# Kernel optimization log

Hardware: AMD Instinct MI355X
Metric: run time of the kernel (lower is better)

Reference implementation:

```python
import jax, jax.numpy as jnp
import numpy as np

N_NODES = 50000
N_EDGES = 500000
SQRT3_INV = 1.0 / np.sqrt(3.0).astype(np.float32)  # CG norm for 1e x 1e -> 0e
SQRT2_INV = 1.0 / np.sqrt(2.0).astype(np.float32)  # CG norm for 1e x 1e -> 1e


def setup_inputs() -> dict:
    key = jax.random.key(0)
    k1, k2, k3, k4, k5 = jax.random.split(key, 5)
    X = jax.random.normal(k1, (N_NODES, 128), dtype=jnp.float32)   # 32x0e + 32x1e
    Y = jax.random.normal(k2, (N_EDGES, 4), dtype=jnp.float32)     # 0e + 1e (edge SH)
    W = jax.random.normal(k3, (N_EDGES, 160), dtype=jnp.float32)   # 5 paths x 32 mul
    rows = jax.random.randint(k4, (N_EDGES,), 0, N_NODES, dtype=jnp.int64)  # receivers
    cols = jax.random.randint(k5, (N_EDGES,), 0, N_NODES, dtype=jnp.int64)  # senders
    return {"X": X, "Y": Y, "W": W, "rows": rows, "cols": cols}


def _edge_messages(Xj, Y, W):
    # Xj: [E,128] gathered sender features, Y: [E,4], W: [E,160]
    E = Xj.shape[0]
    x0 = Xj[:, :32]                       # [E,32]   32x0e
    x1 = Xj[:, 32:].reshape(E, 32, 3)     # [E,32,3] 32x1e
    y0 = Y[:, 0:1]                        # [E,1]    0e
    y1 = Y[:, 1:4]                        # [E,3]    1e
    w = W.reshape(E, 5, 32)               # per-path uvu weights
    # CG paths (uvu):
    p1 = w[:, 0] * x0 * y0                                     # 0e x 0e -> 0e  [E,32]
    p2 = (w[:, 1] * x0)[:, :, None] * y1[:, None, :]           # 0e x 1e -> 1e  [E,32,3]
    p3 = w[:, 2][:, :, None] * x1 * y0[:, :, None]             # 1e x 0e -> 1e  [E,32,3]
    p4 = w[:, 3] * jnp.einsum('eua,ea->eu', x1, y1) * SQRT3_INV  # 1e x 1e -> 0e [E,32]
    p5 = w[:, 4][:, :, None] * jnp.cross(x1, y1[:, None, :]) * SQRT2_INV  # 1e x 1e -> 1e
    return jnp.concatenate(
        [p1, p2.reshape(E, 96), p3.reshape(E, 96), p4, p5.reshape(E, 96)], axis=1
    )  # [E,352]


def reference(X, Y, W, rows, cols):
    # z_i = sum_{(i,j,e)} W_e (x_j (x)_CG y_e); rows = receiver i, cols = sender j
    Xj = X[cols]                              # per-edge gather [E,128]
    msg = _edge_messages(Xj, Y, W)            # [E,352]
    Z = jax.ops.segment_sum(msg, rows, num_segments=X.shape[0])  # scatter-add
    return Z
```

## Files before the change

### kernel.cpp

```cpp
#include <hip/hip_runtime.h>


#define SQRT3_INV 0.57735026918962576451f
#define SQRT2_INV 0.70710678118654752440f
#define KCAP 128

typedef __attribute__((ext_vector_type(4))) float f4;
typedef __attribute__((ext_vector_type(2))) int   i2;
struct F3 { float a, b, c; };

__global__ void scatter_bin_kernel(const int* __restrict__ rows, const int* __restrict__ cols,
                                   int* __restrict__ cnt, i2* __restrict__ slots,
                                   int* __restrict__ ovf_cnt, int* __restrict__ ovf_list,
                                   int nE) {
    int e = blockIdx.x * blockDim.x + threadIdx.x;
    if (e >= nE) return;
    int r = rows[e];
    int p = atomicAdd(&cnt[r], 1);
    if (p < KCAP) {
        i2 rec; rec.x = e; rec.y = cols[e];
        slots[(size_t)r * KCAP + p] = rec;
    } else {
        int q = atomicAdd(ovf_cnt, 1);
        ovf_list[q] = e;
    }
}

__global__ __launch_bounds__(256) void tpc_gather(
    const float* __restrict__ X,
    const float* __restrict__ Y,
    const float* __restrict__ W,
    const i2* __restrict__ slots,
    const int* __restrict__ cnt,
    float* __restrict__ Z,
    int n_nodes)
{
    int node = blockIdx.x * 8 + (threadIdx.x >> 5);
    if (node >= n_nodes) return;
    int u = threadIdx.x & 31;

    float a1 = 0.f, a2a = 0.f, a2b = 0.f, a2c = 0.f;
    float a3a = 0.f, a3b = 0.f, a3c = 0.f, a4 = 0.f;
    float a5a = 0.f, a5b = 0.f, a5c = 0.f;

    int n = cnt[node];
    if (n > KCAP) n = KCAP;
    const i2* sb = slots + (size_t)node * KCAP;

#define EDGE_BODY(EC_)                                                        \
    do {                                                                      \
        const float* We = W + (size_t)(unsigned)(EC_).x * 160;                \
        const float* Xr = X + (size_t)(unsigned)(EC_).y * 128;                \
        const f4 yv = *reinterpret_cast<const f4*>(Y + (size_t)(unsigned)(EC_).x * 4); \
        const float x0 = Xr[u];                                               \
        const F3 x1 = *reinterpret_cast<const F3*>(Xr + 32 + 3 * u);          \
        const float x1a = x1.a, x1b = x1.b, x1c = x1.c;                       \
        const float y0 = yv.x, y1a = yv.y, y1b = yv.z, y1c = yv.w;            \
        const float w0 = __builtin_nontemporal_load(We + u);                  \
        const float w1 = __builtin_nontemporal_load(We + 32 + u);             \
        const float w2 = __builtin_nontemporal_load(We + 64 + u);             \
        const float w3 = __builtin_nontemporal_load(We + 96 + u);             \
        const float w4 = __builtin_nontemporal_load(We + 128 + u);            \
        a1 += w0 * x0 * y0;                                                   \
        const float w1x0 = w1 * x0;                                           \
        a2a += w1x0 * y1a; a2b += w1x0 * y1b; a2c += w1x0 * y1c;              \
        const float w2y0 = w2 * y0;                                           \
        a3a += w2y0 * x1a; a3b += w2y0 * x1b; a3c += w2y0 * x1c;              \
        const float dot = x1a * y1a + x1b * y1b + x1c * y1c;                  \
        a4 += w3 * dot * SQRT3_INV;                                           \
        const float w4s = w4 * SQRT2_INV;                                     \
        a5a += w4s * (x1b * y1c - x1c * y1b);                                 \
        a5b += w4s * (x1c * y1a - x1a * y1c);                                 \
        a5c += w4s * (x1a * y1b - x1b * y1a);                                 \
    } while (0)

    int i = 0;
    for (; i + 1 < n; i += 2) {
        const i2 ec0 = sb[i];
        const i2 ec1 = sb[i + 1];
        EDGE_BODY(ec0);
        EDGE_BODY(ec1);
    }
    if (i < n) {
        const i2 ec0 = sb[i];
        EDGE_BODY(ec0);
    }
#undef EDGE_BODY

    float* Zr = Z + (size_t)node * 352;
    __builtin_nontemporal_store(a1,  Zr + u);
    __builtin_nontemporal_store(a2a, Zr + 32 + 3 * u + 0);
    __builtin_nontemporal_store(a2b, Zr + 32 + 3 * u + 1);
    __builtin_nontemporal_store(a2c, Zr + 32 + 3 * u + 2);
    __builtin_nontemporal_store(a3a, Zr + 128 + 3 * u + 0);
    __builtin_nontemporal_store(a3b, Zr + 128 + 3 * u + 1);
    __builtin_nontemporal_store(a3c, Zr + 128 + 3 * u + 2);
    __builtin_nontemporal_store(a4,  Zr + 224 + u);
    __builtin_nontemporal_store(a5a, Zr + 256 + 3 * u + 0);
    __builtin_nontemporal_store(a5b, Zr + 256 + 3 * u + 1);
    __builtin_nontemporal_store(a5c, Zr + 256 + 3 * u + 2);
}

__global__ void ovf_kernel(const float* __restrict__ X, const float* __restrict__ Y,
                           const float* __restrict__ W, const int* __restrict__ rows,
                           const int* __restrict__ cols, const int* __restrict__ ovf_cnt,
                           const int* __restrict__ ovf_list, float* __restrict__ Z) {
    const int total = ovf_cnt[0] * 32;
    for (int idx = blockIdx.x * blockDim.x + threadIdx.x; idx < total;
         idx += gridDim.x * blockDim.x) {
        const int e = ovf_list[idx >> 5];
        const int u = idx & 31;
        const int r = rows[e];
        const int c = cols[e];
        const float* Xr = X + (size_t)c * 128;
        const float x0 = Xr[u];
        const float x1a = Xr[32 + 3 * u], x1b = Xr[33 + 3 * u], x1c = Xr[34 + 3 * u];
        const float* Ye = Y + (size_t)e * 4;
        const float y0 = Ye[0], y1a = Ye[1], y1b = Ye[2], y1c = Ye[3];
        const float* We = W + (size_t)e * 160;
        const float w0 = We[u], w1 = We[32 + u], w2 = We[64 + u], w3 = We[96 + u], w4 = We[128 + u];
        const float w1x0 = w1 * x0;
        const float w2y0 = w2 * y0;
        const float dot = x1a * y1a + x1b * y1b + x1c * y1c;
        const float w4s = w4 * SQRT2_INV;
        float* Zr = Z + (size_t)r * 352;
        atomicAdd(&Zr[u], w0 * x0 * y0);
        atomicAdd(&Zr[32 + 3 * u + 0], w1x0 * y1a);
        atomicAdd(&Zr[32 + 3 * u + 1], w1x0 * y1b);
        atomicAdd(&Zr[32 + 3 * u + 2], w1x0 * y1c);
        atomicAdd(&Zr[128 + 3 * u + 0], w2y0 * x1a);
        atomicAdd(&Zr[128 + 3 * u + 1], w2y0 * x1b);
        atomicAdd(&Zr[128 + 3 * u + 2], w2y0 * x1c);
        atomicAdd(&Zr[224 + u], w3 * dot * SQRT3_INV);
        atomicAdd(&Zr[256 + 3 * u + 0], w4s * (x1b * y1c - x1c * y1b));
        atomicAdd(&Zr[256 + 3 * u + 1], w4s * (x1c * y1a - x1a * y1c));
        atomicAdd(&Zr[256 + 3 * u + 2], w4s * (x1a * y1b - x1b * y1a));
    }
}

__global__ __launch_bounds__(256) void tpc_edge_kernel(
    const float* __restrict__ X, const float* __restrict__ Y, const float* __restrict__ W,
    const int* __restrict__ rows, const int* __restrict__ cols, float* __restrict__ Z, int n_edges)
{
    int gid = blockIdx.x * blockDim.x + threadIdx.x;
    int e = gid >> 5;
    int u = gid & 31;
    if (e >= n_edges) return;
    const int r = rows[e];
    const int c = cols[e];
    const float* Xr = X + (size_t)c * 128;
    const float x0 = Xr[u];
    const float x1a = Xr[32 + 3 * u], x1b = Xr[33 + 3 * u], x1c = Xr[34 + 3 * u];
    const float* Ye = Y + (size_t)e * 4;
    const float y0 = Ye[0], y1a = Ye[1], y1b = Ye[2], y1c = Ye[3];
    const float* We = W + (size_t)e * 160;
    const float w0 = We[u], w1 = We[32 + u], w2 = We[64 + u], w3 = We[96 + u], w4 = We[128 + u];
    const float w1x0 = w1 * x0;
    const float w2y0 = w2 * y0;
    const float dot = x1a * y1a + x1b * y1b + x1c * y1c;
    const float w4s = w4 * SQRT2_INV;
    float* Zr = Z + (size_t)r * 352;
    atomicAdd(&Zr[u], w0 * x0 * y0);
    atomicAdd(&Zr[32 + 3 * u + 0], w1x0 * y1a);
    atomicAdd(&Zr[32 + 3 * u + 1], w1x0 * y1b);
    atomicAdd(&Zr[32 + 3 * u + 2], w1x0 * y1c);
    atomicAdd(&Zr[128 + 3 * u + 0], w2y0 * x1a);
    atomicAdd(&Zr[128 + 3 * u + 1], w2y0 * x1b);
    atomicAdd(&Zr[128 + 3 * u + 2], w2y0 * x1c);
    atomicAdd(&Zr[224 + u], w3 * dot * SQRT3_INV);
    atomicAdd(&Zr[256 + 3 * u + 0], w4s * (x1b * y1c - x1c * y1b));
    atomicAdd(&Zr[256 + 3 * u + 1], w4s * (x1c * y1a - x1a * y1c));
    atomicAdd(&Zr[256 + 3 * u + 2], w4s * (x1a * y1b - x1b * y1a));
}

extern "C" void kernel_launch(void* const* d_in, const int* in_sizes, int n_in,
                              void* d_out, int out_size, void* d_ws, size_t ws_size,
                              hipStream_t stream) {
    const float* X    = (const float*)d_in[0];
    const float* Y    = (const float*)d_in[1];
    const float* W    = (const float*)d_in[2];
    const int*   rows = (const int*)d_in[3];
    const int*   cols = (const int*)d_in[4];
    float* Z = (float*)d_out;

    const int n_edges = in_sizes[3];
    const int n_nodes = in_sizes[0] / 128;

    size_t slots_bytes = (size_t)n_nodes * KCAP * sizeof(i2);
    size_t need = slots_bytes + (size_t)(n_nodes + 1 + n_edges) * sizeof(int);
    if (ws_size < need) {
        hipMemsetAsync(d_out, 0, (size_t)out_size * sizeof(float), stream);
        const long long threads_total = (long long)n_edges * 32;
        const int grid = (int)((threads_total + 255) / 256);
        tpc_edge_kernel<<<grid, 256, 0, stream>>>(X, Y, W, rows, cols, Z, n_edges);
        return;
    }

    char* base = (char*)d_ws;
    i2*  slots   = (i2*)base;
    int* cnt     = (int*)(base + slots_bytes);
    int* ovf_cnt = cnt + n_nodes;
    int* ovf_list= ovf_cnt + 1;

    hipMemsetAsync(cnt, 0, (size_t)(n_nodes + 1) * sizeof(int), stream);

    const int gE = (n_edges + 255) / 256;
    scatter_bin_kernel<<<gE, 256, 0, stream>>>(rows, cols, cnt, slots, ovf_cnt, ovf_list, n_edges);

    const int gG = (n_nodes + 7) / 8;
    tpc_gather<<<gG, 256, 0, stream>>>(X, Y, W, slots, cnt, Z, n_nodes);

    ovf_kernel<<<64, 256, 0, stream>>>(X, Y, W, rows, cols, ovf_cnt, ovf_list, Z);
}
```

Measured before the change: 142.4 us.

## Split each node's edges across two half-wavefronts and reduce with shuffles

The gather kernel now assigns a full 64-lane wavefront per node instead of 32 lanes. The two halves process alternating edges and combine their partial sums with a cross-half shuffle before one half writes the output. This doubles the number of in-flight edge loads per node, aiming to hide gather latency on irregular degree lists. KCAP drops from 128 to 64, which shrinks the slot buffer, and the overflow counter is folded into the count array. In exchange, the launch needs twice as many waves and adds a shuffle reduction per output.

```diff
diff --git a/kernel.cpp b/kernel.cpp
--- a/kernel.cpp
+++ b/kernel.cpp
@@ -3,49 +3,11 @@
 
 #define SQRT3_INV 0.57735026918962576451f
 #define SQRT2_INV 0.70710678118654752440f
-#define KCAP 128
+#define KCAP 64
 
 typedef __attribute__((ext_vector_type(4))) float f4;
 typedef __attribute__((ext_vector_type(2))) int   i2;
 struct F3 { float a, b, c; };
-
-__global__ void scatter_bin_kernel(const int* __restrict__ rows, const int* __restrict__ cols,
-                                   int* __restrict__ cnt, i2* __restrict__ slots,
-                                   int* __restrict__ ovf_cnt, int* __restrict__ ovf_list,
-                                   int nE) {
-    int e = blockIdx.x * blockDim.x + threadIdx.x;
-    if (e >= nE) return;
-    int r = rows[e];
-    int p = atomicAdd(&cnt[r], 1);
-    if (p < KCAP) {
-        i2 rec; rec.x = e; rec.y = cols[e];
-        slots[(size_t)r * KCAP + p] = rec;
-    } else {
-        int q = atomicAdd(ovf_cnt, 1);
-        ovf_list[q] = e;
-    }
-}
-
-__global__ __launch_bounds__(256) void tpc_gather(
-    const float* __restrict__ X,
-    const float* __restrict__ Y,
-    const float* __restrict__ W,
-    const i2* __restrict__ slots,
-    const int* __restrict__ cnt,
-    float* __restrict__ Z,
-    int n_nodes)
-{
-    int node = blockIdx.x * 8 + (threadIdx.x >> 5);
-    if (node >= n_nodes) return;
-    int u = threadIdx.x & 31;
-
-    float a1 = 0.f, a2a = 0.f, a2b = 0.f, a2c = 0.f;
-    float a3a = 0.f, a3b = 0.f, a3c = 0.f, a4 = 0.f;
-    float a5a = 0.f, a5b = 0.f, a5c = 0.f;
-
-    int n = cnt[node];
-    if (n > KCAP) n = KCAP;
-    const i2* sb = slots + (size_t)node * KCAP;
 
 #define EDGE_BODY(EC_)                                                        \
     do {                                                                      \
@@ -74,38 +36,91 @@
         a5c += w4s * (x1a * y1b - x1b * y1a);                                 \
     } while (0)
 
+__global__ void scatter_bin_kernel(const int* __restrict__ rows, const int* __restrict__ cols,
+                                   int* __restrict__ cnt, i2* __restrict__ slots,
+                                   int* __restrict__ ovf_list, int n_nodes, int nE) {
+    int e = blockIdx.x * blockDim.x + threadIdx.x;
+    if (e >= nE) return;
+    int r = rows[e];
+    int p = atomicAdd(&cnt[r], 1);
+    if (p < KCAP) {
+        i2 rec; rec.x = e; rec.y = cols[e];
+        slots[(size_t)r * KCAP + p] = rec;
+    } else {
+        int q = atomicAdd(&cnt[n_nodes], 1);
+        ovf_list[q] = e;
+    }
+}
+
+__global__ __launch_bounds__(256) void tpc_gather(
+    const float* __restrict__ X,
+    const float* __restrict__ Y,
+    const float* __restrict__ W,
+    const i2* __restrict__ slots,
+    const int* __restrict__ cnt,
+    float* __restrict__ Z,
+    int n_nodes)
+{
+    int node = blockIdx.x * 4 + (threadIdx.x >> 6);
+    if (node >= n_nodes) return;
+    const int lane = threadIdx.x & 63;
+    const int u    = lane & 31;
+    const int slot = lane >> 5;
+
+    float a1 = 0.f, a2a = 0.f, a2b = 0.f, a2c = 0.f;
+    float a3a = 0.f, a3b = 0.f, a3c = 0.f, a4 = 0.f;
+    float a5a = 0.f, a5b = 0.f, a5c = 0.f;
+
+    int n = cnt[node];
+    if (n > KCAP) n = KCAP;
+    const i2* sb = slots + (size_t)node * KCAP;
+
     int i = 0;
-    for (; i + 1 < n; i += 2) {
-        const i2 ec0 = sb[i];
-        const i2 ec1 = sb[i + 1];
+    for (; i + 3 < n; i += 4) {
+        const i2 ec0 = sb[i + slot];
+        const i2 ec1 = sb[i + 2 + slot];
         EDGE_BODY(ec0);
         EDGE_BODY(ec1);
     }
-    if (i < n) {
-        const i2 ec0 = sb[i];
+    for (; i + slot < n; i += 2) {
+        const i2 ec0 = sb[i + slot];
         EDGE_BODY(ec0);
     }
-#undef EDGE_BODY
-
-    float* Zr = Z + (size_t)node * 352;
-    __builtin_nontemporal_store(a1,  Zr + u);
-    __builtin_nontemporal_store(a2a, Zr + 32 + 3 * u + 0);
-    __builtin_nontemporal_store(a2b, Zr + 32 + 3 * u + 1);
-    __builtin_nontemporal_store(a2c, Zr + 32 + 3 * u + 2);
-    __builtin_nontemporal_store(a3a, Zr + 128 + 3 * u + 0);
-    __builtin_nontemporal_store(a3b, Zr + 128 + 3 * u + 1);
-    __builtin_nontemporal_store(a3c, Zr + 128 + 3 * u + 2);
-    __builtin_nontemporal_store(a4,  Zr + 224 + u);
-    __builtin_nontemporal_store(a5a, Zr + 256 + 3 * u + 0);
-    __builtin_nontemporal_store(a5b, Zr + 256 + 3 * u + 1);
-    __builtin_nontemporal_store(a5c, Zr + 256 + 3 * u + 2);
+
+    a1  += __shfl_xor(a1,  32, 64);
+    a2a += __shfl_xor(a2a, 32, 64);
+    a2b += __shfl_xor(a2b, 32, 64);
+    a2c += __shfl_xor(a2c, 32, 64);
+    a3a += __shfl_xor(a3a, 32, 64);
+    a3b += __shfl_xor(a3b, 32, 64);
+    a3c += __shfl_xor(a3c, 32, 64);
+    a4  += __shfl_xor(a4,  32, 64);
+    a5a += __shfl_xor(a5a, 32, 64);
+    a5b += __shfl_xor(a5b, 32, 64);
+    a5c += __shfl_xor(a5c, 32, 64);
+
+    if (slot == 0) {
+        float* Zr = Z + (size_t)node * 352;
+        __builtin_nontemporal_store(a1,  Zr + u);
+        __builtin_nontemporal_store(a2a, Zr + 32 + 3 * u + 0);
+        __builtin_nontemporal_store(a2b, Zr + 32 + 3 * u + 1);
+        __builtin_nontemporal_store(a2c, Zr + 32 + 3 * u + 2);
+        __builtin_nontemporal_store(a3a, Zr + 128 + 3 * u + 0);
+        __builtin_nontemporal_store(a3b, Zr + 128 + 3 * u + 1);
+        __builtin_nontemporal_store(a3c, Zr + 128 + 3 * u + 2);
+        __builtin_nontemporal_store(a4,  Zr + 224 + u);
+        __builtin_nontemporal_store(a5a, Zr + 256 + 3 * u + 0);
+        __builtin_nontemporal_store(a5b, Zr + 256 + 3 * u + 1);
+        __builtin_nontemporal_store(a5c, Zr + 256 + 3 * u + 2);
+    }
 }
 
 __global__ void ovf_kernel(const float* __restrict__ X, const float* __restrict__ Y,
                            const float* __restrict__ W, const int* __restrict__ rows,
-                           const int* __restrict__ cols, const int* __restrict__ ovf_cnt,
-                           const int* __restrict__ ovf_list, float* __restrict__ Z) {
-    const int total = ovf_cnt[0] * 32;
+                           const int* __restrict__ cols, const int* __restrict__ cnt,
+                           const int* __restrict__ ovf_list, float* __restrict__ Z,
+                           int n_nodes) {
+    const int total = cnt[n_nodes] * 32;
     for (int idx = blockIdx.x * blockDim.x + threadIdx.x; idx < total;
          idx += gridDim.x * blockDim.x) {
         const int e = ovf_list[idx >> 5];
@@ -197,18 +212,17 @@
     }
 
     char* base = (char*)d_ws;
-    i2*  slots   = (i2*)base;
-    int* cnt     = (int*)(base + slots_bytes);
-    int* ovf_cnt = cnt + n_nodes;
-    int* ovf_list= ovf_cnt + 1;
+    i2*  slots    = (i2*)base;
+    int* cnt      = (int*)(base + slots_bytes);
+    int* ovf_list = cnt + n_nodes + 1;
 
     hipMemsetAsync(cnt, 0, (size_t)(n_nodes + 1) * sizeof(int), stream);
 
     const int gE = (n_edges + 255) / 256;
-    scatter_bin_kernel<<<gE, 256, 0, stream>>>(rows, cols, cnt, slots, ovf_cnt, ovf_list, n_edges);
-
-    const int gG = (n_nodes + 7) / 8;
+    scatter_bin_kernel<<<gE, 256, 0, stream>>>(rows, cols, cnt, slots, ovf_list, n_nodes, n_edges);
+
+    const int gG = (n_nodes + 3) / 4;
     tpc_gather<<<gG, 256, 0, stream>>>(X, Y, W, slots, cnt, Z, n_nodes);
 
-    ovf_kernel<<<64, 256, 0, stream>>>(X, Y, W, rows, cols, ovf_cnt, ovf_list, Z);
-}
+    ovf_kernel<<<64, 256, 0, stream>>>(X, Y, W, rows, cols, cnt, ovf_list, Z, n_nodes);
+}
```

New measurement: 138.1 us. -3.1%, faster.
